# Performance work log

Measured on AMD Instinct MI355X. Metric: run time of the kernel, lower is better.

## Reference

```python
import jax, jax.numpy as jnp
import numpy as np

SIZES = [(1362944, 123904), (123904, 11264), (11264, 1024)]  # (n_src, n_tgt) per hop
FANOUT = 10
IN_CH, HID, OUT_CH = 128, 256, 47
BN_EPS = 1e-5


def setup_inputs() -> dict:
    key = jax.random.key(0)
    ks = iter(jax.random.split(key, 64))
    inp = {"x": jax.random.normal(next(ks), (SIZES[0][0], IN_CH), jnp.float32)}
    for i, (ns, nt) in enumerate(SIZES):
        e = nt * FANOUT
        src = jax.random.randint(next(ks), (e,), 0, ns, dtype=jnp.int32)
        tgt = jax.random.randint(next(ks), (e,), 0, nt, dtype=jnp.int32)
        inp[f"ei{i}"] = jnp.stack([src, tgt])  # [2, E]
    dins = [IN_CH, HID, HID]
    for i, din in enumerate(dins):
        inp[f"c{i}_w1"] = jax.random.normal(next(ks), (din, HID), jnp.float32) * (2.0 / din) ** 0.5
        inp[f"c{i}_b1"] = jnp.zeros((HID,), jnp.float32)
        inp[f"c{i}_g"] = jnp.ones((HID,), jnp.float32)
        inp[f"c{i}_be"] = jnp.zeros((HID,), jnp.float32)
        inp[f"c{i}_w2"] = jax.random.normal(next(ks), (HID, HID), jnp.float32) * (2.0 / HID) ** 0.5
        inp[f"c{i}_b2"] = jnp.zeros((HID,), jnp.float32)
    inp["lin1_w"] = jax.random.normal(next(ks), (HID, HID), jnp.float32) * (1.0 / HID) ** 0.5
    inp["lin1_b"] = jnp.zeros((HID,), jnp.float32)
    inp["lin2_w"] = jax.random.normal(next(ks), (HID, OUT_CH), jnp.float32) * (1.0 / HID) ** 0.5
    inp["lin2_b"] = jnp.zeros((OUT_CH,), jnp.float32)
    return inp


def _gin_layer(x, ei, n_tgt, w1, b1, g, be, w2, b2):
    # GINConv(eps=0): h = MLP(x_target + sum_{j->i} x_j)
    x_tgt = x[:n_tgt]
    msg = jax.ops.segment_sum(x[ei[0]], ei[1], num_segments=n_tgt)
    h = x_tgt + msg
    h = h @ w1 + b1
    mu = jnp.mean(h, axis=0)
    var = jnp.var(h, axis=0)  # biased, as in torch BN training mode
    h = (h - mu) * jax.lax.rsqrt(var + BN_EPS) * g + be
    h = jax.nn.relu(h)
    h = jax.nn.relu(h @ w2 + b2)
    return h


def reference(x, ei0, ei1, ei2,
              c0_w1, c0_b1, c0_g, c0_be, c0_w2, c0_b2,
              c1_w1, c1_b1, c1_g, c1_be, c1_w2, c1_b2,
              c2_w1, c2_b1, c2_g, c2_be, c2_w2, c2_b2,
              lin1_w, lin1_b, lin2_w, lin2_b):
    eis = [ei0, ei1, ei2]
    params = [(c0_w1, c0_b1, c0_g, c0_be, c0_w2, c0_b2),
              (c1_w1, c1_b1, c1_g, c1_be, c1_w2, c1_b2),
              (c2_w1, c2_b1, c2_g, c2_be, c2_w2, c2_b2)]
    h = x
    for i, (_, n_tgt) in enumerate(SIZES):
        h = _gin_layer(h, eis[i], n_tgt, *params[i])
    h = jax.nn.relu(h @ lin1_w + lin1_b)
    # dropout(p=0.5) is identity in eval mode
    h = h @ lin2_w + lin2_b
    return jax.nn.log_softmax(h, axis=-1)
```

## Files before the change

kernel.cpp:

```cpp
#include <hip/hip_runtime.h>
#include <cmath>

typedef _Float16 f16;
typedef _Float16 half8 __attribute__((ext_vector_type(8)));
typedef _Float16 half4 __attribute__((ext_vector_type(4)));
typedef float f32x4 __attribute__((ext_vector_type(4)));

__device__ __forceinline__ void atomAddF(float* p, float v) { unsafeAtomicAdd(p, v); }

__device__ __forceinline__ void gload16(const void* g, void* l) {
    __builtin_amdgcn_global_load_lds((const __attribute__((address_space(1))) void*)g,
                                     (__attribute__((address_space(3))) void*)l, 16, 0, 0);
}

struct SetupP {
    const float* ws[7];
    f16* wd[7];
    const float* l2s;
    float* l2d;
    int* deg;
};

__global__ void setup_all(SetupP p) {
    int i = blockIdx.x * 256 + threadIdx.x;
    if (i < 32768) {
        int k = i >> 8, n = i & 255;
        p.wd[0][(size_t)n * 128 + k] = (f16)p.ws[0][i];
        return;
    }
    i -= 32768;
    if (i < 6 * 65536) {
        int m = i >> 16, r = i & 65535;
        int k = r >> 8, n = r & 255;
        p.wd[1 + m][(size_t)n * 256 + k] = (f16)p.ws[1 + m][r];
        return;
    }
    i -= 6 * 65536;
    if (i < 12032) {
        int k = i / 47, j = i - k * 47;
        p.l2d[(size_t)j * 256 + k] = p.l2s[i];
        return;
    }
    i -= 12032;
    if (i < 136192) p.deg[i] = 0;
}

__global__ void zero_stats(float* p) { p[blockIdx.x * 256 + threadIdx.x] = 0.f; }

__global__ void fill_all(const int* __restrict__ e0, const int* __restrict__ e1,
                         const int* __restrict__ e2, int E0, int E1, int E2, int* __restrict__ deg,
                         int* __restrict__ adj) {
    int e = blockIdx.x * 256 + threadIdx.x;
    const int *src, *tgt;
    int* d;
    int* a;
    if (e < E0) {
        src = e0; tgt = e0 + E0; d = deg; a = adj;
    } else if (e < E0 + E1) {
        e -= E0;
        src = e1; tgt = e1 + E1; d = deg + 123904; a = adj + (size_t)123904 * 64;
    } else if (e < E0 + E1 + E2) {
        e -= E0 + E1;
        src = e2; tgt = e2 + E2; d = deg + 135168; a = adj + (size_t)135168 * 64;
    } else {
        return;
    }
    int t = tgt[e];
    int pos = atomicAdd(&d[t], 1);
    if (pos < 64) a[(size_t)t * 64 + pos] = src[e];
}


__global__ void gather128(const float* __restrict__ x, const int* __restrict__ deg,
                          const int* __restrict__ adj, f16* __restrict__ h) {
    const int wave = threadIdx.x >> 6, lane = threadIdx.x & 63;
    const int row = blockIdx.x * 4 + wave;
    const int c = lane * 2;
    const float* xr = x + (size_t)row * 128 + c;
    float a0 = xr[0], a1 = xr[1];
    const int n = min(deg[row], 64);
    const int myadj = adj[(size_t)row * 64 + lane];
    int j = 0;
    for (; j + 4 <= n; j += 4) {
        int s0 = __shfl(myadj, j), s1 = __shfl(myadj, j + 1);
        int s2 = __shfl(myadj, j + 2), s3 = __shfl(myadj, j + 3);
        const float* p0 = x + (size_t)s0 * 128 + c;
        const float* p1 = x + (size_t)s1 * 128 + c;
        const float* p2 = x + (size_t)s2 * 128 + c;
        const float* p3 = x + (size_t)s3 * 128 + c;
        float b00 = p0[0], b01 = p0[1], b10 = p1[0], b11 = p1[1];
        float b20 = p2[0], b21 = p2[1], b30 = p3[0], b31 = p3[1];
        a0 += (b00 + b10) + (b20 + b30);
        a1 += (b01 + b11) + (b21 + b31);
    }
    for (; j < n; ++j) {
        int s = __shfl(myadj, j);
        const float* p = x + (size_t)s * 128 + c;
        a0 += p[0];
        a1 += p[1];
    }
    f16* hp = h + (size_t)row * 128 + c;
    hp[0] = (f16)a0;
    hp[1] = (f16)a1;
}

__global__ void gather256(const f16* __restrict__ x, const int* __restrict__ deg,
                          const int* __restrict__ adj, f16* __restrict__ h) {
    const int wave = threadIdx.x >> 6, lane = threadIdx.x & 63;
    const int row = blockIdx.x * 4 + wave;
    const int c = lane * 4;
    half4 xv = *(const half4*)(x + (size_t)row * 256 + c);
    float a0 = (float)xv[0], a1 = (float)xv[1], a2 = (float)xv[2], a3 = (float)xv[3];
    const int n = min(deg[row], 64);
    const int myadj = adj[(size_t)row * 64 + lane];
    int j = 0;
    for (; j + 4 <= n; j += 4) {
        int s0 = __shfl(myadj, j), s1 = __shfl(myadj, j + 1);
        int s2 = __shfl(myadj, j + 2), s3 = __shfl(myadj, j + 3);
        half4 v0 = *(const half4*)(x + (size_t)s0 * 256 + c);
        half4 v1 = *(const half4*)(x + (size_t)s1 * 256 + c);
        half4 v2 = *(const half4*)(x + (size_t)s2 * 256 + c);
        half4 v3 = *(const half4*)(x + (size_t)s3 * 256 + c);
        a0 += ((float)v0[0] + (float)v1[0]) + ((float)v2[0] + (float)v3[0]);
        a1 += ((float)v0[1] + (float)v1[1]) + ((float)v2[1] + (float)v3[1]);
        a2 += ((float)v0[2] + (float)v1[2]) + ((float)v2[2] + (float)v3[2]);
        a3 += ((float)v0[3] + (float)v1[3]) + ((float)v2[3] + (float)v3[3]);
    }
    for (; j < n; ++j) {
        int s = __shfl(myadj, j);
        half4 v = *(const half4*)(x + (size_t)s * 256 + c);
        a0 += (float)v[0];
        a1 += (float)v[1];
        a2 += (float)v[2];
        a3 += (float)v[3];
    }
    half4 o;
    o[0] = (f16)a0;
    o[1] = (f16)a1;
    o[2] = (f16)a2;
    o[3] = (f16)a3;
    *(half4*)(h + (size_t)row * 256 + c) = o;
}

template <bool RELU>
__global__ __launch_bounds__(256) void gemm128(const f16* __restrict__ A, const f16* __restrict__ Bt,
                                               const float* __restrict__ bias, f16* __restrict__ C,
                                               int M, int N, int K) {
    __shared__ __attribute__((aligned(16))) f16 sA[128 * 32];
    __shared__ __attribute__((aligned(16))) f16 sB[128 * 32];
    const int tid = threadIdx.x;
    const int wave = tid >> 6, lane = tid & 63;
    const int quad = lane >> 4, l16 = lane & 15;
    const int wr = (wave & 1) * 64, wc = (wave >> 1) * 64;
    const int row0 = blockIdx.x * 128, col0 = blockIdx.y * 128;

    const int i0 = tid, i1 = tid + 256;
    const int r0s = i0 >> 2, c0s = (i0 & 3) ^ ((r0s >> 1) & 3);
    const int r1s = i1 >> 2, c1s = (i1 & 3) ^ ((r1s >> 1) & 3);
    const f16* ga0 = A + (size_t)(row0 + r0s) * K + c0s * 8;
    const f16* ga1 = A + (size_t)(row0 + r1s) * K + c1s * 8;
    const f16* gb0 = Bt + (size_t)(col0 + r0s) * K + c0s * 8;
    const f16* gb1 = Bt + (size_t)(col0 + r1s) * K + c1s * 8;
    f16* la0 = &sA[i0 * 8];
    f16* la1 = &sA[i1 * 8];
    f16* lb0 = &sB[i0 * 8];
    f16* lb1 = &sB[i1 * 8];

    f32x4 acc[4][4] = {};

    for (int k0 = 0; k0 < K; k0 += 32) {
        __syncthreads();
        gload16(ga0 + k0, la0);
        gload16(ga1 + k0, la1);
        gload16(gb0 + k0, lb0);
        gload16(gb1 + k0, lb1);
        __syncthreads();
        half8 af[4], bf[4];
#pragma unroll
        for (int r = 0; r < 4; ++r) {
            const int ar = wr + r * 16 + l16;
            af[r] = *(const half8*)&sA[ar * 32 + ((quad ^ ((ar >> 1) & 3)) * 8)];
        }
#pragma unroll
        for (int c = 0; c < 4; ++c) {
            const int br = wc + c * 16 + l16;
            bf[c] = *(const half8*)&sB[br * 32 + ((quad ^ ((br >> 1) & 3)) * 8)];
        }
#pragma unroll
        for (int r = 0; r < 4; ++r)
#pragma unroll
            for (int c = 0; c < 4; ++c)
                acc[r][c] = __builtin_amdgcn_mfma_f32_16x16x32_f16(af[r], bf[c], acc[r][c], 0, 0, 0);
    }

#pragma unroll
    for (int c = 0; c < 4; ++c) {
        const int gcol = col0 + wc + c * 16 + l16;
        const float b = bias[gcol];
#pragma unroll
        for (int r = 0; r < 4; ++r) {
#pragma unroll
            for (int i = 0; i < 4; ++i) {
                const int grow = row0 + wr + r * 16 + quad * 4 + i;
                float v = acc[r][c][i] + b;
                if (RELU) v = fmaxf(v, 0.f);
                C[(size_t)grow * N + gcol] = (f16)v;
            }
        }
    }
}

template <bool RELU>
__global__ __launch_bounds__(256) void gemm_bt(const f16* __restrict__ A, const f16* __restrict__ Bt,
                                               const float* __restrict__ bias, f16* __restrict__ C,
                                               int M, int N, int K) {
    constexpr int BM = 64, BN = 64, BK = 32, LP = 40;
    __shared__ f16 sA[BM * LP];
    __shared__ f16 sB[BN * LP];
    const int tid = threadIdx.x;
    const int wave = tid >> 6, lane = tid & 63;
    const int quad = lane >> 4, l16 = lane & 15;
    const int wr = (wave & 1) * 32, wc = (wave >> 1) * 32;
    const int row0 = blockIdx.x * BM, col0 = blockIdx.y * BN;
    const int srow = tid >> 2, soff = (tid & 3) * 8;

    f32x4 acc[2][2] = {};

    for (int k0 = 0; k0 < K; k0 += BK) {
        __syncthreads();
        *(half8*)&sA[srow * LP + soff] =
            *(const half8*)(A + (size_t)(row0 + srow) * K + (k0 + soff));
        *(half8*)&sB[srow * LP + soff] =
            *(const half8*)(Bt + (size_t)(col0 + srow) * K + (k0 + soff));
        __syncthreads();
        half8 af[2], bf[2];
#pragma unroll
        for (int r = 0; r < 2; ++r) af[r] = *(const half8*)&sA[(wr + r * 16 + l16) * LP + quad * 8];
#pragma unroll
        for (int c = 0; c < 2; ++c) bf[c] = *(const half8*)&sB[(wc + c * 16 + l16) * LP + quad * 8];
#pragma unroll
        for (int r = 0; r < 2; ++r)
#pragma unroll
            for (int c = 0; c < 2; ++c)
                acc[r][c] = __builtin_amdgcn_mfma_f32_16x16x32_f16(af[r], bf[c], acc[r][c], 0, 0, 0);
    }

#pragma unroll
    for (int c = 0; c < 2; ++c) {
        const int gcol = col0 + wc + c * 16 + l16;
        const float b = bias[gcol];
#pragma unroll
        for (int r = 0; r < 2; ++r) {
#pragma unroll
            for (int i = 0; i < 4; ++i) {
                const int grow = row0 + wr + r * 16 + quad * 4 + i;
                float v = acc[r][c][i] + b;
                if (RELU) v = fmaxf(v, 0.f);
                C[(size_t)grow * N + gcol] = (f16)v;
            }
        }
    }
}


__global__ void colstats(const f16* __restrict__ h1, int nt, float* __restrict__ colsum,
                         float* __restrict__ colsumsq) {
    const int c = threadIdx.x;
    const int r0 = blockIdx.x * 128;
    const int rend = min(r0 + 128, nt);
    float s = 0.f, ss = 0.f;
    for (int r = r0; r < rend; ++r) {
        float v = (float)h1[(size_t)r * 256 + c];
        s += v;
        ss += v * v;
    }
    atomAddF(&colsum[c], s);
    atomAddF(&colsumsq[c], ss);
}

__global__ void bn_finalize(const float* __restrict__ colsum, const float* __restrict__ colsumsq,
                            const float* __restrict__ g, const float* __restrict__ be, float nt_inv,
                            float* __restrict__ scale, float* __restrict__ shift) {
    int c = threadIdx.x;
    float mu = colsum[c] * nt_inv;
    float var = colsumsq[c] * nt_inv - mu * mu;
    float sc = g[c] * rsqrtf(var + 1e-5f);
    scale[c] = sc;
    shift[c] = be[c] - mu * sc;
}

__global__ void bn_apply(f16* __restrict__ h, int total8, const float* __restrict__ scale,
                         const float* __restrict__ shift) {
    int i = blockIdx.x * 256 + threadIdx.x;
    if (i >= total8) return;
    size_t base = (size_t)i * 8;
    int c = (int)(base & 255);
    half8 v = *(half8*)(h + base);
#pragma unroll
    for (int j = 0; j < 8; ++j) {
        float f = (float)v[j] * scale[c + j] + shift[c + j];
        v[j] = (f16)fmaxf(f, 0.f);
    }
    *(half8*)(h + base) = v;
}

__global__ void head2(const f16* __restrict__ T, const float* __restrict__ w2t,
                      const float* __restrict__ b2, float* __restrict__ out, int rows) {
    const int row = blockIdx.x;
    const int lane = threadIdx.x;
    __shared__ float tr[256];
    for (int i = lane; i < 256; i += 64) tr[i] = (float)T[(size_t)row * 256 + i];
    __syncthreads();
    float d = -1e30f;
    if (lane < 47) {
        const float* wr = w2t + (size_t)lane * 256;
        float dot = 0.f;
        for (int k = 0; k < 256; k += 4) {
            dot += tr[k] * wr[k] + tr[k + 1] * wr[k + 1] + tr[k + 2] * wr[k + 2] +
                   tr[k + 3] * wr[k + 3];
        }
        d = dot + b2[lane];
    }
    float m = d;
    for (int off = 32; off; off >>= 1) m = fmaxf(m, __shfl_xor(m, off));
    float e = (lane < 47) ? expf(d - m) : 0.f;
    float s = e;
    for (int off = 32; off; off >>= 1) s += __shfl_xor(s, off);
    if (lane < 47) out[(size_t)row * 47 + lane] = d - m - logf(s);
}


extern "C" void kernel_launch(void* const* d_in, const int* in_sizes, int n_in, void* d_out,
                              int out_size, void* d_ws, size_t ws_size, hipStream_t stream) {
    const float* x0 = (const float*)d_in[0];
    const int* ei[3] = {(const int*)d_in[1], (const int*)d_in[2], (const int*)d_in[3]};
    const int E[3] = {in_sizes[1] / 2, in_sizes[2] / 2, in_sizes[3] / 2};
    const float* c_w1[3] = {(const float*)d_in[4], (const float*)d_in[10], (const float*)d_in[16]};
    const float* c_b1[3] = {(const float*)d_in[5], (const float*)d_in[11], (const float*)d_in[17]};
    const float* c_g[3] = {(const float*)d_in[6], (const float*)d_in[12], (const float*)d_in[18]};
    const float* c_be[3] = {(const float*)d_in[7], (const float*)d_in[13], (const float*)d_in[19]};
    const float* c_w2[3] = {(const float*)d_in[8], (const float*)d_in[14], (const float*)d_in[20]};
    const float* c_b2[3] = {(const float*)d_in[9], (const float*)d_in[15], (const float*)d_in[21]};
    const float* lin1_w = (const float*)d_in[22];
    const float* lin1_b = (const float*)d_in[23];
    const float* lin2_w = (const float*)d_in[24];
    const float* lin2_b = (const float*)d_in[25];
    float* out = (float*)d_out;

    const int NT[3] = {123904, 11264, 1024};

    char* base = (char*)d_ws;
    size_t off = 0;
    auto take = [&](size_t bytes) -> char* {
        char* p = base + off;
        off = (off + bytes + 255) & ~(size_t)255;
        return p;
    };
    f16* w1t[3];
    w1t[0] = (f16*)take((size_t)256 * 128 * sizeof(f16));
    w1t[1] = (f16*)take((size_t)256 * 256 * sizeof(f16));
    w1t[2] = (f16*)take((size_t)256 * 256 * sizeof(f16));
    f16* w2t[3];
    for (int i = 0; i < 3; ++i) w2t[i] = (f16*)take((size_t)256 * 256 * sizeof(f16));
    f16* lin1t = (f16*)take((size_t)256 * 256 * sizeof(f16));
    float* lin2t_ = (float*)take((size_t)47 * 256 * sizeof(float));
    float* stats = (float*)take(1024 * sizeof(float));
    int* deg = (int*)take((size_t)136192 * sizeof(int));
    int* adj = (int*)take((size_t)136192 * 64 * sizeof(int));
    f16* h0 = (f16*)take((size_t)123904 * 128 * sizeof(f16));
    f16* h1 = (f16*)take((size_t)123904 * 256 * sizeof(f16));
    f16* X1 = (f16*)take((size_t)123904 * 256 * sizeof(f16));
    f16* X2 = (f16*)take((size_t)11264 * 256 * sizeof(f16));
    f16* X3 = (f16*)take((size_t)1024 * 256 * sizeof(f16));
    f16* T = (f16*)take((size_t)1024 * 256 * sizeof(f16));
    (void)ws_size;
    (void)out_size;
    (void)n_in;

    int* deg_l[3] = {deg, deg + 123904, deg + 135168};
    int* adj_l[3] = {adj, adj + (size_t)123904 * 64, adj + (size_t)135168 * 64};

    SetupP sp;
    sp.ws[0] = c_w1[0];
    sp.ws[1] = c_w1[1];
    sp.ws[2] = c_w1[2];
    sp.ws[3] = c_w2[0];
    sp.ws[4] = c_w2[1];
    sp.ws[5] = c_w2[2];
    sp.ws[6] = lin1_w;
    sp.wd[0] = w1t[0];
    sp.wd[1] = w1t[1];
    sp.wd[2] = w1t[2];
    sp.wd[3] = w2t[0];
    sp.wd[4] = w2t[1];
    sp.wd[5] = w2t[2];
    sp.wd[6] = lin1t;
    sp.l2s = lin2_w;
    sp.l2d = lin2t_;
    sp.deg = deg;
    setup_all<<<(574208 + 255) / 256, 256, 0, stream>>>(sp);

    fill_all<<<(E[0] + E[1] + E[2] + 255) / 256, 256, 0, stream>>>(ei[0], ei[1], ei[2], E[0], E[1],
                                                                  E[2], deg, adj);

    auto bn_mid = [&](const float* g, const float* be, int nt) {
        zero_stats<<<2, 256, 0, stream>>>(stats);
        colstats<<<(nt + 127) / 128, 256, 0, stream>>>(h1, nt, stats, stats + 256);
        bn_finalize<<<1, 256, 0, stream>>>(stats, stats + 256, g, be, 1.0f / nt, stats + 512,
                                           stats + 768);
        bn_apply<<<(nt * 256 / 8 + 255) / 256, 256, 0, stream>>>(h1, nt * 256 / 8, stats + 512,
                                                                 stats + 768);
    };

    gather128<<<NT[0] / 4, 256, 0, stream>>>(x0, deg_l[0], adj_l[0], h0);
    gemm128<false><<<dim3(NT[0] / 128, 2), 256, 0, stream>>>(h0, w1t[0], c_b1[0], h1, NT[0], 256,
                                                             128);
    bn_mid(c_g[0], c_be[0], NT[0]);
    gemm128<true><<<dim3(NT[0] / 128, 2), 256, 0, stream>>>(h1, w2t[0], c_b2[0], X1, NT[0], 256,
                                                            256);

    gather256<<<NT[1] / 4, 256, 0, stream>>>(X1, deg_l[1], adj_l[1], h0);
    gemm128<false><<<dim3(NT[1] / 128, 2), 256, 0, stream>>>(h0, w1t[1], c_b1[1], h1, NT[1], 256,
                                                             256);
    bn_mid(c_g[1], c_be[1], NT[1]);
    gemm128<true><<<dim3(NT[1] / 128, 2), 256, 0, stream>>>(h1, w2t[1], c_b2[1], X2, NT[1], 256,
                                                            256);

    gather256<<<NT[2] / 4, 256, 0, stream>>>(X2, deg_l[2], adj_l[2], h0);
    gemm_bt<false><<<dim3(NT[2] / 64, 4), 256, 0, stream>>>(h0, w1t[2], c_b1[2], h1, NT[2], 256,
                                                            256);
    bn_mid(c_g[2], c_be[2], NT[2]);
    gemm_bt<true><<<dim3(NT[2] / 64, 4), 256, 0, stream>>>(h1, w2t[2], c_b2[2], X3, NT[2], 256,
                                                           256);

    gemm_bt<true><<<dim3(16, 4), 256, 0, stream>>>(X3, lin1t, lin1_b, T, 1024, 256, 256);
    head2<<<1024, 64, 0, stream>>>(T, lin2t_, lin2_b, out, 1024);
}
```

Measured before the change: 1.302 ms.

## Fuse BatchNorm stats into GEMM1 epilogue and BN apply into GEMM2 prologue

Column sum and sum-of-squares are now accumulated in the first GEMM's epilogue, using wave shuffles, shared-memory atomics and global atomics. The BN finalize plus scale/shift/ReLU step is folded into the A-operand load of the second GEMM. This removes the separate zero_stats, colstats, bn_finalize and bn_apply kernels and their extra passes over h1. The stats buffers are zeroed in the setup kernel. In exchange, the A load of the second GEMM goes through registers instead of direct global-to-LDS loads, which adds ALU work and a dependency before each tile is stored to LDS. The stats are taken from the pre-rounding fp32 values instead of the stored fp16.

Result: faster. 1.191 ms (-8.5%).

```diff
diff --git a/kernel.cpp b/kernel.cpp
--- a/kernel.cpp
+++ b/kernel.cpp
@@ -18,6 +18,7 @@
     f16* wd[7];
     const float* l2s;
     float* l2d;
+    float* stats;
     int* deg;
 };
 
@@ -42,10 +43,13 @@
         return;
     }
     i -= 12032;
+    if (i < 1536) {
+        p.stats[i] = 0.f;
+        return;
+    }
+    i -= 1536;
     if (i < 136192) p.deg[i] = 0;
 }
-
-__global__ void zero_stats(float* p) { p[blockIdx.x * 256 + threadIdx.x] = 0.f; }
 
 __global__ void fill_all(const int* __restrict__ e0, const int* __restrict__ e1,
                          const int* __restrict__ e2, int E0, int E1, int E2, int* __restrict__ deg,
@@ -142,17 +146,26 @@
     *(half4*)(h + (size_t)row * 256 + c) = o;
 }
 
-template <bool RELU>
-__global__ __launch_bounds__(256) void gemm128(const f16* __restrict__ A, const f16* __restrict__ Bt,
-                                               const float* __restrict__ bias, f16* __restrict__ C,
-                                               int M, int N, int K) {
+__global__ __launch_bounds__(256) void gemm128_stats(const f16* __restrict__ A,
+                                                     const f16* __restrict__ Bt,
+                                                     const float* __restrict__ bias,
+                                                     f16* __restrict__ C,
+                                                     float* __restrict__ colsum,
+                                                     float* __restrict__ colsumsq, int M, int N,
+                                                     int K) {
     __shared__ __attribute__((aligned(16))) f16 sA[128 * 32];
     __shared__ __attribute__((aligned(16))) f16 sB[128 * 32];
+    __shared__ float ssum[128], ssq[128];
     const int tid = threadIdx.x;
     const int wave = tid >> 6, lane = tid & 63;
     const int quad = lane >> 4, l16 = lane & 15;
     const int wr = (wave & 1) * 64, wc = (wave >> 1) * 64;
     const int row0 = blockIdx.x * 128, col0 = blockIdx.y * 128;
+
+    if (tid < 128)
+        ssum[tid] = 0.f;
+    else
+        ssq[tid - 128] = 0.f;
 
     const int i0 = tid, i1 = tid + 256;
     const int r0s = i0 >> 2, c0s = (i0 & 3) ^ ((r0s >> 1) & 3);
@@ -195,15 +208,123 @@
 
 #pragma unroll
     for (int c = 0; c < 4; ++c) {
-        const int gcol = col0 + wc + c * 16 + l16;
+        const int lcol = wc + c * 16 + l16;
+        const int gcol = col0 + lcol;
         const float b = bias[gcol];
+        float cs = 0.f, cq = 0.f;
 #pragma unroll
         for (int r = 0; r < 4; ++r) {
 #pragma unroll
             for (int i = 0; i < 4; ++i) {
                 const int grow = row0 + wr + r * 16 + quad * 4 + i;
                 float v = acc[r][c][i] + b;
-                if (RELU) v = fmaxf(v, 0.f);
+                C[(size_t)grow * N + gcol] = (f16)v;
+                cs += v;
+                cq += v * v;
+            }
+        }
+        cs += __shfl_xor(cs, 16);
+        cs += __shfl_xor(cs, 32);
+        cq += __shfl_xor(cq, 16);
+        cq += __shfl_xor(cq, 32);
+        if (quad == 0) {
+            atomicAdd(&ssum[lcol], cs);
+            atomicAdd(&ssq[lcol], cq);
+        }
+    }
+    __syncthreads();
+    if (tid < 128)
+        atomAddF(&colsum[col0 + tid], ssum[tid]);
+    else
+        atomAddF(&colsumsq[col0 + tid - 128], ssq[tid - 128]);
+}
+
+__global__ __launch_bounds__(256) void gemm128_bn(const f16* __restrict__ A,
+                                                  const f16* __restrict__ Bt,
+                                                  const float* __restrict__ bias,
+                                                  const float* __restrict__ colsum,
+                                                  const float* __restrict__ colsumsq,
+                                                  const float* __restrict__ g,
+                                                  const float* __restrict__ be, float nt_inv,
+                                                  f16* __restrict__ C, int M, int N, int K) {
+    __shared__ __attribute__((aligned(16))) f16 sA[128 * 32];
+    __shared__ __attribute__((aligned(16))) f16 sB[128 * 32];
+    __shared__ float s_scale[256], s_shift[256];
+    const int tid = threadIdx.x;
+    const int wave = tid >> 6, lane = tid & 63;
+    const int quad = lane >> 4, l16 = lane & 15;
+    const int wr = (wave & 1) * 64, wc = (wave >> 1) * 64;
+    const int row0 = blockIdx.x * 128, col0 = blockIdx.y * 128;
+
+    {
+        float mu = colsum[tid] * nt_inv;
+        float var = colsumsq[tid] * nt_inv - mu * mu;
+        float sc = g[tid] * rsqrtf(var + 1e-5f);
+        s_scale[tid] = sc;
+        s_shift[tid] = be[tid] - mu * sc;
+    }
+    __syncthreads();
+
+    const int i0 = tid, i1 = tid + 256;
+    const int r0s = i0 >> 2, c0s = (i0 & 3) ^ ((r0s >> 1) & 3);
+    const int r1s = i1 >> 2, c1s = (i1 & 3) ^ ((r1s >> 1) & 3);
+    const f16* ga0 = A + (size_t)(row0 + r0s) * K + c0s * 8;
+    const f16* ga1 = A + (size_t)(row0 + r1s) * K + c1s * 8;
+    const f16* gb0 = Bt + (size_t)(col0 + r0s) * K + c0s * 8;
+    const f16* gb1 = Bt + (size_t)(col0 + r1s) * K + c1s * 8;
+    f16* la0 = &sA[i0 * 8];
+    f16* la1 = &sA[i1 * 8];
+    f16* lb0 = &sB[i0 * 8];
+    f16* lb1 = &sB[i1 * 8];
+
+    f32x4 acc[4][4] = {};
+
+    for (int k0 = 0; k0 < K; k0 += 32) {
+        half8 va0 = *(const half8*)(ga0 + k0);
+        half8 va1 = *(const half8*)(ga1 + k0);
+        half8 ta0, ta1;
+        const int kb0 = k0 + c0s * 8, kb1 = k0 + c1s * 8;
+#pragma unroll
+        for (int j = 0; j < 8; ++j) {
+            float f0 = (float)va0[j] * s_scale[kb0 + j] + s_shift[kb0 + j];
+            ta0[j] = (f16)fmaxf(f0, 0.f);
+            float f1 = (float)va1[j] * s_scale[kb1 + j] + s_shift[kb1 + j];
+            ta1[j] = (f16)fmaxf(f1, 0.f);
+        }
+        __syncthreads();
+        gload16(gb0 + k0, lb0);
+        gload16(gb1 + k0, lb1);
+        *(half8*)la0 = ta0;
+        *(half8*)la1 = ta1;
+        __syncthreads();
+        half8 af[4], bf[4];
+#pragma unroll
+        for (int r = 0; r < 4; ++r) {
+            const int ar = wr + r * 16 + l16;
+            af[r] = *(const half8*)&sA[ar * 32 + ((quad ^ ((ar >> 1) & 3)) * 8)];
+        }
+#pragma unroll
+        for (int c = 0; c < 4; ++c) {
+            const int br = wc + c * 16 + l16;
+            bf[c] = *(const half8*)&sB[br * 32 + ((quad ^ ((br >> 1) & 3)) * 8)];
+        }
+#pragma unroll
+        for (int r = 0; r < 4; ++r)
+#pragma unroll
+            for (int c = 0; c < 4; ++c)
+                acc[r][c] = __builtin_amdgcn_mfma_f32_16x16x32_f16(af[r], bf[c], acc[r][c], 0, 0, 0);
+    }
+
+#pragma unroll
+    for (int c = 0; c < 4; ++c) {
+        const int gcol = col0 + wc + c * 16 + l16;
+        const float b = bias[gcol];
+#pragma unroll
+        for (int r = 0; r < 4; ++r) {
+#pragma unroll
+            for (int i = 0; i < 4; ++i) {
+                const int grow = row0 + wr + r * 16 + quad * 4 + i;
+                float v = fmaxf(acc[r][c][i] + b, 0.f);
                 C[(size_t)grow * N + gcol] = (f16)v;
             }
         }
@@ -260,48 +381,6 @@
             }
         }
     }
-}
-
-
-__global__ void colstats(const f16* __restrict__ h1, int nt, float* __restrict__ colsum,
-                         float* __restrict__ colsumsq) {
-    const int c = threadIdx.x;
-    const int r0 = blockIdx.x * 128;
-    const int rend = min(r0 + 128, nt);
-    float s = 0.f, ss = 0.f;
-    for (int r = r0; r < rend; ++r) {
-        float v = (float)h1[(size_t)r * 256 + c];
-        s += v;
-        ss += v * v;
-    }
-    atomAddF(&colsum[c], s);
-    atomAddF(&colsumsq[c], ss);
-}
-
-__global__ void bn_finalize(const float* __restrict__ colsum, const float* __restrict__ colsumsq,
-                            const float* __restrict__ g, const float* __restrict__ be, float nt_inv,
-                            float* __restrict__ scale, float* __restrict__ shift) {
-    int c = threadIdx.x;
-    float mu = colsum[c] * nt_inv;
-    float var = colsumsq[c] * nt_inv - mu * mu;
-    float sc = g[c] * rsqrtf(var + 1e-5f);
-    scale[c] = sc;
-    shift[c] = be[c] - mu * sc;
-}
-
-__global__ void bn_apply(f16* __restrict__ h, int total8, const float* __restrict__ scale,
-                         const float* __restrict__ shift) {
-    int i = blockIdx.x * 256 + threadIdx.x;
-    if (i >= total8) return;
-    size_t base = (size_t)i * 8;
-    int c = (int)(base & 255);
-    half8 v = *(half8*)(h + base);
-#pragma unroll
-    for (int j = 0; j < 8; ++j) {
-        float f = (float)v[j] * scale[c + j] + shift[c + j];
-        v[j] = (f16)fmaxf(f, 0.f);
-    }
-    *(half8*)(h + base) = v;
 }
 
 __global__ void head2(const f16* __restrict__ T, const float* __restrict__ w2t,
@@ -364,7 +443,7 @@
     for (int i = 0; i < 3; ++i) w2t[i] = (f16*)take((size_t)256 * 256 * sizeof(f16));
     f16* lin1t = (f16*)take((size_t)256 * 256 * sizeof(f16));
     float* lin2t_ = (float*)take((size_t)47 * 256 * sizeof(float));
-    float* stats = (float*)take(1024 * sizeof(float));
+    float* stats = (float*)take(3 * 512 * sizeof(float));
     int* deg = (int*)take((size_t)136192 * sizeof(int));
     int* adj = (int*)take((size_t)136192 * 64 * sizeof(int));
     f16* h0 = (f16*)take((size_t)123904 * 128 * sizeof(f16));
@@ -379,6 +458,7 @@
 
     int* deg_l[3] = {deg, deg + 123904, deg + 135168};
     int* adj_l[3] = {adj, adj + (size_t)123904 * 64, adj + (size_t)135168 * 64};
+    float* cs_l[3] = {stats, stats + 512, stats + 1024};
 
     SetupP sp;
     sp.ws[0] = c_w1[0];
@@ -397,41 +477,33 @@
     sp.wd[6] = lin1t;
     sp.l2s = lin2_w;
     sp.l2d = lin2t_;
+    sp.stats = stats;
     sp.deg = deg;
-    setup_all<<<(574208 + 255) / 256, 256, 0, stream>>>(sp);
+    setup_all<<<2249, 256, 0, stream>>>(sp);
 
     fill_all<<<(E[0] + E[1] + E[2] + 255) / 256, 256, 0, stream>>>(ei[0], ei[1], ei[2], E[0], E[1],
                                                                   E[2], deg, adj);
 
-    auto bn_mid = [&](const float* g, const float* be, int nt) {
-        zero_stats<<<2, 256, 0, stream>>>(stats);
-        colstats<<<(nt + 127) / 128, 256, 0, stream>>>(h1, nt, stats, stats + 256);
-        bn_finalize<<<1, 256, 0, stream>>>(stats, stats + 256, g, be, 1.0f / nt, stats + 512,
-                                           stats + 768);
-        bn_apply<<<(nt * 256 / 8 + 255) / 256, 256, 0, stream>>>(h1, nt * 256 / 8, stats + 512,
-                                                                 stats + 768);
-    };
-
     gather128<<<NT[0] / 4, 256, 0, stream>>>(x0, deg_l[0], adj_l[0], h0);
-    gemm128<false><<<dim3(NT[0] / 128, 2), 256, 0, stream>>>(h0, w1t[0], c_b1[0], h1, NT[0], 256,
-                                                             128);
-    bn_mid(c_g[0], c_be[0], NT[0]);
-    gemm128<true><<<dim3(NT[0] / 128, 2), 256, 0, stream>>>(h1, w2t[0], c_b2[0], X1, NT[0], 256,
-                                                            256);
+    gemm128_stats<<<dim3(NT[0] / 128, 2), 256, 0, stream>>>(h0, w1t[0], c_b1[0], h1, cs_l[0],
+                                                            cs_l[0] + 256, NT[0], 256, 128);
+    gemm128_bn<<<dim3(NT[0] / 128, 2), 256, 0, stream>>>(h1, w2t[0], c_b2[0], cs_l[0],
+                                                         cs_l[0] + 256, c_g[0], c_be[0],
+                                                         1.0f / NT[0], X1, NT[0], 256, 256);
 
     gather256<<<NT[1] / 4, 256, 0, stream>>>(X1, deg_l[1], adj_l[1], h0);
-    gemm128<false><<<dim3(NT[1] / 128, 2), 256, 0, stream>>>(h0, w1t[1], c_b1[1], h1, NT[1], 256,
-                                                             256);
-    bn_mid(c_g[1], c_be[1], NT[1]);
-    gemm128<true><<<dim3(NT[1] / 128, 2), 256, 0, stream>>>(h1, w2t[1], c_b2[1], X2, NT[1], 256,
-                                                            256);
+    gemm128_stats<<<dim3(NT[1] / 128, 2), 256, 0, stream>>>(h0, w1t[1], c_b1[1], h1, cs_l[1],
+                                                            cs_l[1] + 256, NT[1], 256, 256);
+    gemm128_bn<<<dim3(NT[1] / 128, 2), 256, 0, stream>>>(h1, w2t[1], c_b2[1], cs_l[1],
+                                                         cs_l[1] + 256, c_g[1], c_be[1],
+                                                         1.0f / NT[1], X2, NT[1], 256, 256);
 
     gather256<<<NT[2] / 4, 256, 0, stream>>>(X2, deg_l[2], adj_l[2], h0);
-    gemm_bt<false><<<dim3(NT[2] / 64, 4), 256, 0, stream>>>(h0, w1t[2], c_b1[2], h1, NT[2], 256,
-                                                            256);
-    bn_mid(c_g[2], c_be[2], NT[2]);
-    gemm_bt<true><<<dim3(NT[2] / 64, 4), 256, 0, stream>>>(h1, w2t[2], c_b2[2], X3, NT[2], 256,
-                                                           256);
+    gemm128_stats<<<dim3(NT[2] / 128, 2), 256, 0, stream>>>(h0, w1t[2], c_b1[2], h1, cs_l[2],
+                                                            cs_l[2] + 256, NT[2], 256, 256);
+    gemm128_bn<<<dim3(NT[2] / 128, 2), 256, 0, stream>>>(h1, w2t[2], c_b2[2], cs_l[2],
+                                                         cs_l[2] + 256, c_g[2], c_be[2],
+                                                         1.0f / NT[2], X3, NT[2], 256, 256);
 
     gemm_bt<true><<<dim3(16, 4), 256, 0, stream>>>(X3, lin1t, lin1_b, T, 1024, 256, 256);
     head2<<<1024, 64, 0, stream>>>(T, lin2t_, lin2_b, out, 1024);
```
